# Performance work log

Measured on AMD Instinct MI355X. Metric: run time of the kernel, lower is better.

The kernel has to match this reference:

```python
import jax, jax.numpy as jnp
import numpy as np
from jax import lax

KS = 3
N = KS * KS  # 9 sampling locations per output pixel


def conv2d(x, w, b, pad, dil=1):
    out = lax.conv_general_dilated(
        x, w, window_strides=(1, 1), padding=((pad, pad), (pad, pad)),
        rhs_dilation=(dil, dil), dimension_numbers=('NCHW', 'OIHW', 'NCHW'))
    return out + b[None, :, None, None]


def deform_conv(x, p_w, p_b, dw, db):
    # Pure deform-conv-v2 semantics: offsets from p_conv, bilinear gather on
    # zero-padded input, then 3x3 contraction over the 9 gathered samples.
    B, C, H, W = x.shape
    offset = conv2d(x, p_w, p_b, 1)                       # (B, 2N, H, W)
    xp = jnp.pad(x, ((0, 0), (0, 0), (1, 1), (1, 1)))     # zero pad by 1
    Hp, Wp = H + 2, W + 2
    rr = jnp.arange(-(KS // 2), KS // 2 + 1)
    pi, pj = jnp.meshgrid(rr, rr, indexing='ij')
    p_n = jnp.concatenate([pi.reshape(-1), pj.reshape(-1)]).astype(x.dtype)   # (2N,)
    gi, gj = jnp.meshgrid(jnp.arange(1, H + 1), jnp.arange(1, W + 1), indexing='ij')
    p0 = jnp.concatenate([jnp.broadcast_to(gi, (N, H, W)),
                          jnp.broadcast_to(gj, (N, H, W))], 0).astype(x.dtype)  # (2N,H,W)
    p = p0[None] + p_n[None, :, None, None] + offset      # (B, 2N, H, W)
    p = jnp.transpose(p, (0, 2, 3, 1))                    # (B, H, W, 2N)
    py, px = p[..., :N], p[..., N:]
    fy, fx = jnp.floor(py), jnp.floor(px)
    lt_y = jnp.clip(fy, 0, Hp - 1); lt_x = jnp.clip(fx, 0, Wp - 1)
    rb_y = jnp.clip(fy + 1, 0, Hp - 1); rb_x = jnp.clip(fx + 1, 0, Wp - 1)
    pyc = jnp.clip(py, 0, Hp - 1); pxc = jnp.clip(px, 0, Wp - 1)
    g_lt = (1 + (lt_y - pyc)) * (1 + (lt_x - pxc))
    g_rb = (1 - (rb_y - pyc)) * (1 - (rb_x - pxc))
    g_lb = (1 + (lt_y - pyc)) * (1 - (rb_x - pxc))
    g_rt = (1 - (rb_y - pyc)) * (1 + (lt_x - pxc))
    xf = xp.reshape(B, C, Hp * Wp)

    def gather(qy, qx):
        idx = (qy.astype(jnp.int32) * Wp + qx.astype(jnp.int32)).reshape(B, -1)
        g = jax.vmap(lambda xb, ib: jnp.take(xb, ib, axis=1))(xf, idx)
        return g.reshape(B, C, H, W, N)

    x_lt = gather(lt_y, lt_x); x_rb = gather(rb_y, rb_x)
    x_lb = gather(lt_y, rb_x); x_rt = gather(rb_y, lt_x)
    samples = (g_lt[:, None] * x_lt + g_rb[:, None] * x_rb
               + g_lb[:, None] * x_lb + g_rt[:, None] * x_rt)  # (B,C,H,W,N)
    out = jnp.einsum('bchwn,ocn->bohw', samples, dw.reshape(dw.shape[0], C, N))
    return out + db[None, :, None, None]


def reference(x, w1, b1, w2, b2, w3, b3, w4, b4, p_w, p_b, dw, db, cw, cb):
    branches = [(w1, b1, 1, 1.0), (w2, b2, 3, 3.0), (w3, b3, 5, 5.0), (w4, b4, 7, 7.0)]
    feats = [deform_conv(conv2d(x, w, b, d, d) * s, p_w, p_b, dw, db)
             for (w, b, d, s) in branches]
    combined = jnp.concatenate(feats, axis=1)             # (B, 4*Cout, H, W)
    return jax.nn.relu(conv2d(combined, cw, cb, 0))


def setup_inputs() -> dict:
    B, Cin, Cout, H, W = 4, 128, 64, 128, 128
    key = jax.random.key(0)
    ks = jax.random.split(key, 16)
    sc3 = 1.0 / np.sqrt(Cin * 9)      # fan-in scale for 3x3 convs
    sc1 = 1.0 / np.sqrt(4 * Cout)     # fan-in scale for 1x1 fuse conv
    scd = 1.0 / np.sqrt(Cout * 9)     # deform main conv
    inp = {'x': jax.random.normal(ks[0], (B, Cin, H, W), jnp.float32)}
    for i in range(4):
        inp[f'w{i+1}'] = jax.random.normal(ks[1 + i], (Cout, Cin, 3, 3), jnp.float32) * sc3
        inp[f'b{i+1}'] = jax.random.normal(ks[5 + i], (Cout,), jnp.float32) * 0.01
    inp['p_w'] = jax.random.normal(ks[9], (2 * N, Cout, 3, 3), jnp.float32) * 0.01
    inp['p_b'] = jax.random.normal(ks[10], (2 * N,), jnp.float32) * 0.01
    inp['dw'] = jax.random.normal(ks[11], (Cout, Cout, 3, 3), jnp.float32) * scd
    inp['db'] = jax.random.normal(ks[12], (Cout,), jnp.float32) * 0.01
    inp['cw'] = jax.random.normal(ks[13], (Cout, 4 * Cout, 1, 1), jnp.float32) * sc1
    inp['cb'] = jax.random.normal(ks[14], (Cout,), jnp.float32) * 0.01
    return inp
```

## Files before the change

kernel.cpp:

```cpp
#include <hip/hip_runtime.h>
#include <hip/hip_bf16.h>

#define H 128
#define W 128
#define CIN 128
#define COUT 64
#define HW (H*W)
#define XW 130
#define FSL (XW*XW*64)
#define XTD 144

typedef __hip_bfloat16 bf16;
typedef __attribute__((ext_vector_type(8)))  short s16x8;
typedef __attribute__((ext_vector_type(16))) float f32x16;

__device__ __forceinline__ float b2f(bf16 v){ return __bfloat162float(v); }
__device__ __forceinline__ bf16  f2b(float v){ return __float2bfloat16(v); }
__device__ __forceinline__ unsigned pack2(float a, float b){
    unsigned short ua = __builtin_bit_cast(unsigned short, f2b(a));
    unsigned short ub = __builtin_bit_cast(unsigned short, f2b(b));
    return (unsigned)ua | ((unsigned)ub << 16);
}
__device__ __forceinline__ unsigned short b16u(float v){
    return __builtin_bit_cast(unsigned short, f2b(v));
}
__device__ __forceinline__ float2 up2(unsigned u){
    float lo = __builtin_bit_cast(float, u << 16);
    float hi = __builtin_bit_cast(float, u & 0xFFFF0000u);
    return make_float2(lo, hi);
}

__global__ __launch_bounds__(256) void k_prep(
    const float* __restrict__ w1, const float* __restrict__ w2,
    const float* __restrict__ w3, const float* __restrict__ w4,
    const float* __restrict__ dw, const float* __restrict__ cw,
    const float* __restrict__ pw,
    uint4* __restrict__ xt4, unsigned* __restrict__ wbt,
    unsigned* __restrict__ dwb2, unsigned* __restrict__ cwb2,
    unsigned* __restrict__ pwb)
{
    int bid = blockIdx.x;
    int t = threadIdx.x;
    if (bid < 1024){
        const int n4 = (4*XTD*XTD*64)/4;
        for (int i = bid*256 + t; i < n4; i += 1024*256)
            xt4[i] = make_uint4(0,0,0,0);
    } else if (bid < 1600){
        int tid = (bid-1024)*256 + t;
        int cpl = tid & 7;
        int oc  = (tid >> 3) & 63;
        int tap = (tid >> 9) % 9;
        int cg  = (tid / 4608) & 7;
        int d   = tid / 36864;
        const float* wt = (d==0)?w1:(d==1)?w2:(d==2)?w3:w4;
        int c = cg*8 + cpl;
        wbt[tid] = pack2(wt[((size_t)oc*CIN + 2*c  )*9 + tap],
                         wt[((size_t)oc*CIN + 2*c+1)*9 + tap]);
    } else if (bid < 1672){
        int i = (bid-1600)*256 + t;
        int n = i>>11, oc = (i>>5)&63, cp = i&31;
        dwb2[i] = pack2(dw[((size_t)oc*64 + 2*cp  )*9 + n],
                        dw[((size_t)oc*64 + 2*cp+1)*9 + n]);
    } else if (bid < 1704){
        int i = (bid-1672)*256 + t;
        int oc = i>>7, cp = i&127;
        cwb2[i] = pack2(cw[(size_t)oc*256 + 2*cp], cw[(size_t)oc*256 + 2*cp+1]);
    } else {
        int i = (bid-1704)*256 + t;
        int cl = i & 3, oc = (i>>2)&31, hf = (i>>7)&1, cq = (i>>8)&3, tap = i>>10;
        int c = cq*16 + hf*8 + cl*2;
        unsigned v = 0u;
        if (oc < 18)
            v = pack2(pw[((size_t)oc*64 + c  )*9 + tap],
                      pw[((size_t)oc*64 + c+1)*9 + tap]);
        pwb[i] = v;
    }
}

__global__ __launch_bounds__(256) void k_xprep(
    const float* __restrict__ x, unsigned* __restrict__ xt)
{
    int y = blockIdx.x, b = blockIdx.y;
    int t = threadIdx.x;
    __shared__ float xsm[64*131];
    for (int ci0 = 0; ci0 < 128; ci0 += 64){
        for (int i=0;i<32;i++){
            int idx = t + 256*i;
            int col = idx & 127, ci = idx >> 7;
            xsm[ci*131 + col] = x[(((size_t)b*CIN + ci0+ci)*H + y)*W + col];
        }
        __syncthreads();
        for (int i=0;i<16;i++){
            int idx = t + 256*i;
            int cpg = idx & 31, col = idx >> 5;
            int cgg = (ci0 >> 4) + (cpg >> 3);
            int cpl = cpg & 7;
            unsigned u = pack2(xsm[(2*cpg)*131 + col], xsm[(2*cpg+1)*131 + col]);
            xt[((((size_t)b*8 + cgg)*XTD + y+8)*XTD + col+8)*8 + cpl] = u;
        }
        __syncthreads();
    }
}

__global__ __launch_bounds__(256,2) void k_branch_mfma(
    const unsigned* __restrict__ xt, const unsigned* __restrict__ wbt,
    const float* __restrict__ b1, const float* __restrict__ b2,
    const float* __restrict__ b3, const float* __restrict__ b4,
    bf16* __restrict__ feats2)
{
    int bid = blockIdx.x;
    int xcd = bid & 7;
    int j   = bid >> 3;
    int zb  = xcd + 8*(j & 1);
    int hp  = j >> 1;
    int d = zb >> 2, b = zb & 3;
    int dil = 2*d + 1;
    int h0 = hp*2;
    const float* bs = (d==0)?b1:(d==1)?b2:(d==2)?b3:b4;
    const float scale = (float)dil;

    __shared__ unsigned smem[10368 + 6912];
    unsigned* As = smem;
    unsigned* Bs = smem + 10368;
    const unsigned short* As16 = (const unsigned short*)As;
    const unsigned short* Bs16 = (const unsigned short*)Bs;

    int t = threadIdx.x;
    int lane = t & 63;
    int w = t >> 6;
    int l31 = lane & 31;
    int half = lane >> 5;

    bf16* fb = feats2 + (size_t)zb*FSL;
    if (t < 32){
        int yy = h0 + 1 + (t>>4);
        int side = (t>>3)&1;
        int q = t & 7;
        uint4 z = make_uint4(0,0,0,0);
        *(uint4*)((unsigned short*)fb + ((size_t)yy*XW + side*129)*64 + q*8) = z;
    }
    if (hp == 0){
        uint4 z = make_uint4(0,0,0,0);
        for (int i=t; i<2080; i+=256){
            int row = i / 1040;
            int r = i % 1040;
            int xx = r >> 3, q = r & 7;
            *(uint4*)((unsigned short*)fb + ((size_t)(row*129)*XW + xx)*64 + q*8) = z;
        }
    }

    f32x16 acc[2][2];
    #pragma unroll
    for (int i=0;i<2;i++)
      #pragma unroll
      for (int jj=0;jj<2;jj++)
        #pragma unroll
        for (int e=0;e<16;e++) acc[i][jj][e] = 0.f;

    const unsigned* xtb_b = xt + (size_t)b*8*XTD*XTD*8;
    int r = w >> 1;
    int pxb = (w & 1) * 64;

    for (int cg=0; cg<8; cg++){
        const unsigned* xs_cg = xtb_b + (size_t)cg*XTD*XTD*8;
        #pragma unroll
        for (int i=0;i<7;i++){
            int idx4 = t + 256*i;
            if (idx4 < 1728){
                int cp4 = idx4 & 1;
                int s   = (idx4 >> 1) % 144;
                int row6= idx4 / 288;
                int ky = row6 >> 1, rr = row6 & 1;
                int yy = h0 + rr + (ky-1)*dil + 8;
                uint4 v = *(const uint4*)(xs_cg + ((size_t)yy*XTD + (s + 8 - dil))*8 + cp4*4);
                *(uint4*)&As[(row6*144 + s)*12 + cp4*4] = v;
            }
        }
        const unsigned* wb_cg = wbt + ((size_t)d*8 + cg)*4608;
        #pragma unroll
        for (int i=0;i<5;i++){
            int idx4 = t + 256*i;
            if (idx4 < 1152){
                int cp4 = idx4 & 1;
                int oc  = (idx4 >> 1) & 63;
                int tap = idx4 >> 7;
                uint4 v = *(const uint4*)(wb_cg + ((size_t)tap*64 + oc)*8 + cp4*4);
                *(uint4*)&Bs[(tap*64 + oc)*12 + cp4*4] = v;
            }
        }
        __syncthreads();
        #pragma unroll
        for (int tap=0; tap<9; tap++){
            int ky = tap/3, kx = tap%3;
            int rowb = (ky*2 + r)*144;
            s16x8 a0 = *(const s16x8*)(As16 + (rowb + pxb      + l31 + kx*dil)*24 + half*8);
            s16x8 a1 = *(const s16x8*)(As16 + (rowb + pxb + 32 + l31 + kx*dil)*24 + half*8);
            s16x8 bb0 = *(const s16x8*)(Bs16 + (tap*64      + l31)*24 + half*8);
            s16x8 bb1 = *(const s16x8*)(Bs16 + (tap*64 + 32 + l31)*24 + half*8);
            acc[0][0] = __builtin_amdgcn_mfma_f32_32x32x16_bf16(a0, bb0, acc[0][0], 0,0,0);
            acc[0][1] = __builtin_amdgcn_mfma_f32_32x32x16_bf16(a0, bb1, acc[0][1], 0,0,0);
            acc[1][0] = __builtin_amdgcn_mfma_f32_32x32x16_bf16(a1, bb0, acc[1][0], 0,0,0);
            acc[1][1] = __builtin_amdgcn_mfma_f32_32x32x16_bf16(a1, bb1, acc[1][1], 0,0,0);
        }
        __syncthreads();
    }

    unsigned short* ep = (unsigned short*)smem;
    float bias0 = bs[l31], bias1 = bs[32 + l31];
    #pragma unroll
    for (int i=0;i<2;i++){
      #pragma unroll
      for (int jj=0;jj<2;jj++){
        int oc = jj*32 + l31;
        float bj = jj ? bias1 : bias0;
        #pragma unroll
        for (int rg=0; rg<4; rg++){
            int m0 = 64*w + 32*i + 8*rg + 4*half;
            #pragma unroll
            for (int e=0;e<4;e++)
                ep[(m0+e)*64 + oc] = b16u((acc[i][jj][4*rg+e] + bj)*scale);
        }
      }
    }
    __syncthreads();
    {
        int row = t >> 7, pxm = t & 127;
        unsigned short* drow = (unsigned short*)fb + ((size_t)(h0+1+row)*XW + pxm + 1)*64;
        const unsigned short* srow = ep + t*64;
        #pragma unroll
        for (int q=0;q<8;q++)
            *(uint4*)(drow + q*8) = *(const uint4*)(srow + q*8);
    }
}

__global__ __launch_bounds__(256,2) void k_offset_mfma(
    const bf16* __restrict__ feats2,
    const unsigned* __restrict__ pwb,
    const float* __restrict__ pb,
    bf16* __restrict__ offs)
{
    int bid = blockIdx.x;
    int xcd  = bid & 7;
    int h    = (bid >> 3) & 127;
    int pass = bid >> 10;
    int zb   = xcd + 8*pass;

    int t = threadIdx.x;
    int lane = t & 63, w = t >> 6;
    int l31 = lane & 31, half = lane >> 5;

    __shared__ unsigned short xs[3*132*68];

    const unsigned short* fin = (const unsigned short*)(feats2 + (size_t)zb*FSL);
    for (int i=t; i<3120; i+=256){
        int row = i / 1040;
        int r   = i % 1040;
        int col = r >> 3, q = r & 7;
        uint4 v = *(const uint4*)(fin + ((size_t)(h+row)*XW + col)*64 + q*8);
        *(uint4*)&xs[(row*132 + col)*68 + q*8] = v;
    }
    __syncthreads();

    f32x16 acc;
    #pragma unroll
    for (int e=0;e<16;e++) acc[e] = 0.f;

    int pxw = 32*w + l31;
    #pragma unroll
    for (int tap=0; tap<9; tap++){
        int ky = tap/3, kx = tap%3;
        const unsigned short* arow = &xs[(ky*132 + pxw + kx)*68 + half*8];
        const unsigned* brow = pwb + (((size_t)tap*4)*2 + half)*128 + l31*4;
        #pragma unroll
        for (int cq=0; cq<4; cq++){
            s16x8 a  = *(const s16x8*)(arow + cq*16);
            s16x8 b0 = *(const s16x8*)(brow + cq*256);
            acc = __builtin_amdgcn_mfma_f32_32x32x16_bf16(a, b0, acc, 0,0,0);
        }
    }
    __syncthreads();

    unsigned short* ep = (unsigned short*)xs;
    if (l31 < 18){
        float bias = pb[l31];
        #pragma unroll
        for (int rg=0; rg<4; rg++){
            int m0 = 32*w + 4*half + 8*rg;
            #pragma unroll
            for (int e=0;e<4;e++)
                ep[l31*132 + m0+e] = b16u(acc[4*rg+e] + bias);
        }
    }
    __syncthreads();
    unsigned short* obase = (unsigned short*)(offs + (size_t)zb*18*HW) ;
    for (int i=t; i<288; i+=256){
        int oc = i >> 4, sg = i & 15;
        *(uint4*)(obase + (size_t)oc*HW + h*W + sg*8) = *(const uint4*)(ep + oc*132 + sg*8);
    }
}

__global__ __launch_bounds__(256,4) void k_deform_mfma(
    const bf16* __restrict__ feats2,
    const bf16* __restrict__ offs,
    const unsigned* __restrict__ dwb2,
    const float* __restrict__ db,
    bf16* __restrict__ dout2)
{
    int bid = blockIdx.x;
    int xcd  = bid & 7;
    int h    = (bid >> 3) & 127;
    int pass = bid >> 10;
    int zb   = xcd + 8*pass;

    int t = threadIdx.x;
    int lane = t & 63, w = t >> 6;
    int l31 = lane & 31, half = lane >> 5;
    int pxg = t >> 3;
    int cq  = t & 7;
    int sub_w = cq >> 1;
    int hf8   = cq & 1;

    #define AROW 516
    __shared__ unsigned smem_d[8*AROW + 2304 + 1024];
    unsigned* Asu = smem_d;
    unsigned* Bsu = smem_d + 8*AROW;
    unsigned* Cd  = smem_d + 8*AROW + 2304;

    const bf16* obase = offs + (size_t)zb*18*HW + h*W;
    const unsigned short* fbase = (const unsigned short*)(feats2 + (size_t)zb*FSL);

    f32x16 acc0, acc1;
    #pragma unroll
    for (int e=0;e<16;e++){ acc0[e]=0.f; acc1[e]=0.f; }

    for (int n=0; n<9; n++){
        const uint4* dsrc = (const uint4*)(dwb2 + n*2048);
        #pragma unroll
        for (int i=0;i<2;i++){
            int j = t + 256*i;
            int idx4 = j*4;
            int oc = idx4 >> 5, cp = idx4 & 31;
            *(uint4*)&Bsu[oc*36 + cp] = dsrc[j];
        }
        if (t < 128){
            float offy = b2f(obase[n*HW + t]);
            float offx = b2f(obase[(n+9)*HW + t]);
            float py  = (float)(h + n/3) + offy;
            float pxf = (float)(t + n%3) + offx;
            float fy = floorf(py), fx = floorf(pxf);
            float lty = fminf(fmaxf(fy,     0.f),129.f);
            float ltx = fminf(fmaxf(fx,     0.f),129.f);
            float rby = fminf(fmaxf(fy+1.f, 0.f),129.f);
            float rbx = fminf(fmaxf(fx+1.f, 0.f),129.f);
            float pyc = fminf(fmaxf(py,     0.f),129.f);
            float pxc = fminf(fmaxf(pxf,    0.f),129.f);
            float ay = 1.f + (lty-pyc), by = 1.f - (rby-pyc);
            float ax = 1.f + (ltx-pxc), bx = 1.f - (rbx-pxc);
            unsigned* cp = &Cd[t*8];
            cp[0] = __builtin_bit_cast(unsigned, ay*ax);
            cp[1] = __builtin_bit_cast(unsigned, ay*bx);
            cp[2] = __builtin_bit_cast(unsigned, by*ax);
            cp[3] = __builtin_bit_cast(unsigned, by*bx);
            cp[4] = (unsigned)(((int)lty*XW + (int)ltx)*64);
            cp[5] = (unsigned)(((int)rbx - (int)ltx)*64);
            cp[6] = (unsigned)(((int)rby - (int)lty)*XW*64);
        }
        __syncthreads();
        #pragma unroll
        for (int s=0; s<4; s++){
            int px = s*32 + pxg;
            const unsigned* cp = &Cd[px*8];
            uint4 c0 = *(const uint4*)cp;
            uint4 c1 = *(const uint4*)(cp + 4);
            float glt = __builtin_bit_cast(float, c0.x);
            float glb = __builtin_bit_cast(float, c0.y);
            float grt = __builtin_bit_cast(float, c0.z);
            float grb = __builtin_bit_cast(float, c0.w);
            int base = (int)c1.x;
            int dxo  = (int)c1.y;
            int dyo  = (int)c1.z;

            const unsigned short* fc = fbase + base + cq*8;
            unsigned LT[4], LB[4], RT[4], RB[4];
            *(uint4*)LT = *(const uint4*)(fc);
            *(uint4*)LB = *(const uint4*)(fc+dxo);
            *(uint4*)RT = *(const uint4*)(fc+dyo);
            *(uint4*)RB = *(const uint4*)(fc+dyo+dxo);
            unsigned pk[4];
            #pragma unroll
            for (int jq=0;jq<4;jq++){
                float2 a = up2(LT[jq]), bq = up2(LB[jq]);
                float2 c = up2(RT[jq]), dq = up2(RB[jq]);
                float slo = glt*a.x + glb*bq.x + grt*c.x + grb*dq.x;
                float shi = glt*a.y + glb*bq.y + grt*c.y + grb*dq.y;
                pk[jq] = pack2(slo, shi);
            }
            uint4 av; av.x=pk[0]; av.y=pk[1]; av.z=pk[2]; av.w=pk[3];
            *(uint4*)&Asu[(sub_w*2 + hf8)*AROW + px*4] = av;
        }
        __syncthreads();
        const unsigned short* As16 = (const unsigned short*)Asu;
        const unsigned short* Bs16 = (const unsigned short*)Bsu;
        #pragma unroll
        for (int s=0;s<4;s++){
            s16x8 a  = *(const s16x8*)(As16 + (s*2+half)*(AROW*2) + (32*w + l31)*8);
            s16x8 b0 = *(const s16x8*)(Bs16 + (l31*36 + s*8 + half*4)*2);
            s16x8 b1 = *(const s16x8*)(Bs16 + ((32+l31)*36 + s*8 + half*4)*2);
            acc0 = __builtin_amdgcn_mfma_f32_32x32x16_bf16(a, b0, acc0, 0,0,0);
            acc1 = __builtin_amdgcn_mfma_f32_32x32x16_bf16(a, b1, acc1, 0,0,0);
        }
        __syncthreads();
    }

    unsigned short* ep = (unsigned short*)smem_d;
    #pragma unroll
    for (int nt=0; nt<2; nt++){
        int oc = nt*32 + l31;
        float bias = db[oc];
        const f32x16& A = nt ? acc1 : acc0;
        #pragma unroll
        for (int rg=0; rg<4; rg++){
            int m0 = 32*w + 4*half + 8*rg;
            #pragma unroll
            for (int e=0;e<4;e++)
                ep[(m0+e)*64 + oc] = b16u(A[4*rg+e] + bias);
        }
    }
    __syncthreads();
    uint4* dst = (uint4*)((unsigned short*)dout2 + ((size_t)zb*128 + h)*(128*64));
    #pragma unroll
    for (int i=0;i<4;i++)
        dst[t + 256*i] = ((const uint4*)ep)[t + 256*i];
    #undef AROW
}

__global__ __launch_bounds__(256,2) void k_combine_mfma(
    const bf16* __restrict__ dout2,
    const unsigned* __restrict__ cwb2,
    const float* __restrict__ cb,
    float* __restrict__ out)
{
    int h = blockIdx.x, b = blockIdx.y;
    int t = threadIdx.x;
    int px = t & 127, hf = t >> 7;
    int lane = t & 63, w = t >> 6, l31 = lane & 31, half = lane >> 5;

    __shared__ unsigned Bsu[64*132];
    __shared__ unsigned Asu2[1024];

    for (int i=t; i<8192; i+=256){
        int oc = i>>7, cp = i&127;
        Bsu[oc*132 + cp] = cwb2[i];
    }
    f32x16 acc0, acc1;
    #pragma unroll
    for (int e=0;e<16;e++){ acc0[e]=0.f; acc1[e]=0.f; }

    const unsigned short* dbase0 = (const unsigned short*)dout2;
    size_t rowsel = ((size_t)b*128 + h)*128 + px;
    uint4 v = *(const uint4*)(dbase0 + rowsel*64 + hf*8);
    for (int kc=0; kc<16; kc++){
        *(uint4*)&Asu2[(hf*128+px)*4] = v;
        __syncthreads();
        if (kc < 15){
            int kn = kc+1;
            int d = kn>>2, c16 = kn&3;
            v = *(const uint4*)(dbase0 + ((size_t)d*4*128*128*64 + rowsel*64) + c16*16 + hf*8);
        }
        const unsigned short* As16 = (const unsigned short*)Asu2;
        const unsigned short* Bs16 = (const unsigned short*)Bsu;
        s16x8 a  = *(const s16x8*)(As16 + (half*128 + 32*w + l31)*8);
        s16x8 b0 = *(const s16x8*)(Bs16 + (l31*132 + kc*8 + half*4)*2);
        s16x8 b1 = *(const s16x8*)(Bs16 + ((32+l31)*132 + kc*8 + half*4)*2);
        acc0 = __builtin_amdgcn_mfma_f32_32x32x16_bf16(a, b0, acc0, 0,0,0);
        acc1 = __builtin_amdgcn_mfma_f32_32x32x16_bf16(a, b1, acc1, 0,0,0);
        __syncthreads();
    }
    float* ep = (float*)Bsu;
    #pragma unroll
    for (int nt=0; nt<2; nt++){
        int oc = nt*32 + l31;
        float bias = cb[oc];
        const f32x16& A = nt ? acc1 : acc0;
        #pragma unroll
        for (int rg=0; rg<4; rg++){
            int m0 = 32*w + 4*half + 8*rg;
            #pragma unroll
            for (int e=0;e<4;e++)
                ep[oc*132 + m0+e] = fmaxf(A[4*rg+e] + bias, 0.f);
        }
    }
    __syncthreads();
    for (int i=t; i<2048; i+=256){
        int oc = i>>5, sg = i&31;
        *(uint4*)&out[(((size_t)b*64+oc)*128 + h)*128 + sg*4] = *(const uint4*)&ep[oc*132 + sg*4];
    }
}

extern "C" void kernel_launch(void* const* d_in, const int* in_sizes, int n_in,
                              void* d_out, int out_size, void* d_ws, size_t ws_size,
                              hipStream_t stream) {
    const float* x  = (const float*)d_in[0];
    const float* w1 = (const float*)d_in[1];
    const float* b1 = (const float*)d_in[2];
    const float* w2 = (const float*)d_in[3];
    const float* b2 = (const float*)d_in[4];
    const float* w3 = (const float*)d_in[5];
    const float* b3 = (const float*)d_in[6];
    const float* w4 = (const float*)d_in[7];
    const float* b4 = (const float*)d_in[8];
    const float* pw = (const float*)d_in[9];
    const float* pb = (const float*)d_in[10];
    const float* dw = (const float*)d_in[11];
    const float* db = (const float*)d_in[12];
    const float* cw = (const float*)d_in[13];
    const float* cb = (const float*)d_in[14];
    float* out = (float*)d_out;

    bf16* feats2 = (bf16*)d_ws;
    bf16* offs   = feats2 + (size_t)16*FSL;
    bf16* region2 = offs + (size_t)16*18*HW;
    bf16* dout2  = region2;
    unsigned* xt  = (unsigned*)region2;
    unsigned* wbt = xt + (size_t)4*8*XTD*XTD*8;
    unsigned* dwb2 = (unsigned*)(dout2 + (size_t)16*128*128*64);
    unsigned* cwb2 = dwb2 + 18432;
    unsigned* pwb  = cwb2 + 8192;

    k_prep        <<<dim3(1740),    256, 0, stream>>>(w1,w2,w3,w4, dw, cw, pw,
                                                      (uint4*)xt, wbt, dwb2, cwb2, pwb);
    k_xprep       <<<dim3(128,4),   256, 0, stream>>>(x, xt);
    k_branch_mfma <<<dim3(1024),    256, 0, stream>>>(xt, wbt, b1,b2,b3,b4, feats2);
    k_offset_mfma <<<dim3(2048),    256, 0, stream>>>(feats2, pwb, pb, offs);
    k_deform_mfma <<<dim3(2048),    256, 0, stream>>>(feats2, offs, dwb2, db, dout2);
    k_combine_mfma<<<dim3(128,4),   256, 0, stream>>>(dout2, cwb2, cb, out);
}
```

Baseline: 316.3 us.

## Pipeline deform gather: double-buffer coords, prefetch corners, read weights from global

The deform-conv kernel now computes the bilinear coordinates for the next tap into a second LDS buffer while the current tap is processed. This removes one barrier per tap. Corner loads for the next 32-pixel slice are issued before blending the current one, and the blend uses packed two-wide float math. The MFMA B operand is read straight from global memory instead of being staged in LDS, which cuts LDS use and a store pass but relies on cache for weight reuse and adds register pressure.

```diff
diff --git a/kernel.cpp b/kernel.cpp
--- a/kernel.cpp
+++ b/kernel.cpp
@@ -13,6 +13,7 @@
 typedef __hip_bfloat16 bf16;
 typedef __attribute__((ext_vector_type(8)))  short s16x8;
 typedef __attribute__((ext_vector_type(16))) float f32x16;
+typedef __attribute__((ext_vector_type(2)))  float f32x2;
 
 __device__ __forceinline__ float b2f(bf16 v){ return __bfloat162float(v); }
 __device__ __forceinline__ bf16  f2b(float v){ return __float2bfloat16(v); }
@@ -28,6 +29,12 @@
     float lo = __builtin_bit_cast(float, u << 16);
     float hi = __builtin_bit_cast(float, u & 0xFFFF0000u);
     return make_float2(lo, hi);
+}
+__device__ __forceinline__ f32x2 up2v(unsigned u){
+    f32x2 r;
+    r.x = __builtin_bit_cast(float, u << 16);
+    r.y = __builtin_bit_cast(float, u & 0xFFFF0000u);
+    return r;
 }
 
 __global__ __launch_bounds__(256) void k_prep(
@@ -299,6 +306,31 @@
     }
 }
 
+__device__ __forceinline__ void deform_coords(
+    const bf16* __restrict__ obase, int h, int n, int px, unsigned* cp)
+{
+    float offy = b2f(obase[n*HW + px]);
+    float offx = b2f(obase[(n+9)*HW + px]);
+    float py  = (float)(h + n/3) + offy;
+    float pxf = (float)(px + n%3) + offx;
+    float fy = floorf(py), fx = floorf(pxf);
+    float lty = fminf(fmaxf(fy,     0.f),129.f);
+    float ltx = fminf(fmaxf(fx,     0.f),129.f);
+    float rby = fminf(fmaxf(fy+1.f, 0.f),129.f);
+    float rbx = fminf(fmaxf(fx+1.f, 0.f),129.f);
+    float pyc = fminf(fmaxf(py,     0.f),129.f);
+    float pxc = fminf(fmaxf(pxf,    0.f),129.f);
+    float ay = 1.f + (lty-pyc), by = 1.f - (rby-pyc);
+    float ax = 1.f + (ltx-pxc), bx = 1.f - (rbx-pxc);
+    cp[0] = __builtin_bit_cast(unsigned, ay*ax);
+    cp[1] = __builtin_bit_cast(unsigned, ay*bx);
+    cp[2] = __builtin_bit_cast(unsigned, by*ax);
+    cp[3] = __builtin_bit_cast(unsigned, by*bx);
+    cp[4] = (unsigned)(((int)lty*XW + (int)ltx)*64);
+    cp[5] = (unsigned)(((int)rbx - (int)ltx)*64);
+    cp[6] = (unsigned)(((int)rby - (int)lty)*XW*64);
+}
+
 __global__ __launch_bounds__(256,4) void k_deform_mfma(
     const bf16* __restrict__ feats2,
     const bf16* __restrict__ offs,
@@ -321,10 +353,9 @@
     int hf8   = cq & 1;
 
     #define AROW 516
-    __shared__ unsigned smem_d[8*AROW + 2304 + 1024];
+    __shared__ unsigned smem_d[8*AROW + 2048];
     unsigned* Asu = smem_d;
-    unsigned* Bsu = smem_d + 8*AROW;
-    unsigned* Cd  = smem_d + 8*AROW + 2304;
+    unsigned* Cd  = smem_d + 8*AROW;
 
     const bf16* obase = offs + (size_t)zb*18*HW + h*W;
     const unsigned short* fbase = (const unsigned short*)(feats2 + (size_t)zb*FSL);
@@ -333,79 +364,78 @@
     #pragma unroll
     for (int e=0;e<16;e++){ acc0[e]=0.f; acc1[e]=0.f; }
 
+    if (t < 128) deform_coords(obase, h, 0, t, &Cd[t*8]);
+    __syncthreads();
+
+    unsigned LTv[2][4], LBv[2][4], RTv[2][4], RBv[2][4];
+    float wg[2][4];
+
     for (int n=0; n<9; n++){
-        const uint4* dsrc = (const uint4*)(dwb2 + n*2048);
-        #pragma unroll
-        for (int i=0;i<2;i++){
-            int j = t + 256*i;
-            int idx4 = j*4;
-            int oc = idx4 >> 5, cp = idx4 & 31;
-            *(uint4*)&Bsu[oc*36 + cp] = dsrc[j];
-        }
-        if (t < 128){
-            float offy = b2f(obase[n*HW + t]);
-            float offx = b2f(obase[(n+9)*HW + t]);
-            float py  = (float)(h + n/3) + offy;
-            float pxf = (float)(t + n%3) + offx;
-            float fy = floorf(py), fx = floorf(pxf);
-            float lty = fminf(fmaxf(fy,     0.f),129.f);
-            float ltx = fminf(fmaxf(fx,     0.f),129.f);
-            float rby = fminf(fmaxf(fy+1.f, 0.f),129.f);
-            float rbx = fminf(fmaxf(fx+1.f, 0.f),129.f);
-            float pyc = fminf(fmaxf(py,     0.f),129.f);
-            float pxc = fminf(fmaxf(pxf,    0.f),129.f);
-            float ay = 1.f + (lty-pyc), by = 1.f - (rby-pyc);
-            float ax = 1.f + (ltx-pxc), bx = 1.f - (rbx-pxc);
-            unsigned* cp = &Cd[t*8];
-            cp[0] = __builtin_bit_cast(unsigned, ay*ax);
-            cp[1] = __builtin_bit_cast(unsigned, ay*bx);
-            cp[2] = __builtin_bit_cast(unsigned, by*ax);
-            cp[3] = __builtin_bit_cast(unsigned, by*bx);
-            cp[4] = (unsigned)(((int)lty*XW + (int)ltx)*64);
-            cp[5] = (unsigned)(((int)rbx - (int)ltx)*64);
-            cp[6] = (unsigned)(((int)rby - (int)lty)*XW*64);
-        }
-        __syncthreads();
-        #pragma unroll
-        for (int s=0; s<4; s++){
-            int px = s*32 + pxg;
-            const unsigned* cp = &Cd[px*8];
+        const unsigned* Cdc = Cd + (n&1)*1024;
+        unsigned*       Cdn = Cd + ((n+1)&1)*1024;
+
+        {
+            const unsigned* cp = &Cdc[(pxg)*8];
             uint4 c0 = *(const uint4*)cp;
             uint4 c1 = *(const uint4*)(cp + 4);
-            float glt = __builtin_bit_cast(float, c0.x);
-            float glb = __builtin_bit_cast(float, c0.y);
-            float grt = __builtin_bit_cast(float, c0.z);
-            float grb = __builtin_bit_cast(float, c0.w);
-            int base = (int)c1.x;
-            int dxo  = (int)c1.y;
-            int dyo  = (int)c1.z;
-
-            const unsigned short* fc = fbase + base + cq*8;
-            unsigned LT[4], LB[4], RT[4], RB[4];
-            *(uint4*)LT = *(const uint4*)(fc);
-            *(uint4*)LB = *(const uint4*)(fc+dxo);
-            *(uint4*)RT = *(const uint4*)(fc+dyo);
-            *(uint4*)RB = *(const uint4*)(fc+dyo+dxo);
+            wg[0][0] = __builtin_bit_cast(float, c0.x);
+            wg[0][1] = __builtin_bit_cast(float, c0.y);
+            wg[0][2] = __builtin_bit_cast(float, c0.z);
+            wg[0][3] = __builtin_bit_cast(float, c0.w);
+            int dxo = (int)c1.y, dyo = (int)c1.z;
+            const unsigned short* fc = fbase + (int)c1.x + cq*8;
+            *(uint4*)&LTv[0][0] = *(const uint4*)(fc);
+            *(uint4*)&LBv[0][0] = *(const uint4*)(fc+dxo);
+            *(uint4*)&RTv[0][0] = *(const uint4*)(fc+dyo);
+            *(uint4*)&RBv[0][0] = *(const uint4*)(fc+dyo+dxo);
+        }
+        if (n < 8 && t < 128) deform_coords(obase, h, n+1, t, &Cdn[t*8]);
+
+        #pragma unroll
+        for (int s=0; s<4; s++){
+            const int par = s & 1;
+            if (s < 3){
+                const int nx = par ^ 1;
+                const unsigned* cp = &Cdc[((s+1)*32+pxg)*8];
+                uint4 c0 = *(const uint4*)cp;
+                uint4 c1 = *(const uint4*)(cp + 4);
+                wg[nx][0] = __builtin_bit_cast(float, c0.x);
+                wg[nx][1] = __builtin_bit_cast(float, c0.y);
+                wg[nx][2] = __builtin_bit_cast(float, c0.z);
+                wg[nx][3] = __builtin_bit_cast(float, c0.w);
+                int dxo = (int)c1.y, dyo = (int)c1.z;
+                const unsigned short* fc = fbase + (int)c1.x + cq*8;
+                *(uint4*)&LTv[nx][0] = *(const uint4*)(fc);
+                *(uint4*)&LBv[nx][0] = *(const uint4*)(fc+dxo);
+                *(uint4*)&RTv[nx][0] = *(const uint4*)(fc+dyo);
+                *(uint4*)&RBv[nx][0] = *(const uint4*)(fc+dyo+dxo);
+            }
+            f32x2 wlt = {wg[par][0], wg[par][0]};
+            f32x2 wlb = {wg[par][1], wg[par][1]};
+            f32x2 wrt = {wg[par][2], wg[par][2]};
+            f32x2 wrb = {wg[par][3], wg[par][3]};
             unsigned pk[4];
             #pragma unroll
-            for (int jq=0;jq<4;jq++){
-                float2 a = up2(LT[jq]), bq = up2(LB[jq]);
-                float2 c = up2(RT[jq]), dq = up2(RB[jq]);
-                float slo = glt*a.x + glb*bq.x + grt*c.x + grb*dq.x;
-                float shi = glt*a.y + glb*bq.y + grt*c.y + grb*dq.y;
-                pk[jq] = pack2(slo, shi);
+            for (int jq=0; jq<4; jq++){
+                f32x2 r = wlt * up2v(LTv[par][jq]);
+                r += wlb * up2v(LBv[par][jq]);
+                r += wrt * up2v(RTv[par][jq]);
+                r += wrb * up2v(RBv[par][jq]);
+                pk[jq] = pack2(r.x, r.y);
             }
+            int px = s*32 + pxg;
             uint4 av; av.x=pk[0]; av.y=pk[1]; av.z=pk[2]; av.w=pk[3];
             *(uint4*)&Asu[(sub_w*2 + hf8)*AROW + px*4] = av;
         }
         __syncthreads();
+
         const unsigned short* As16 = (const unsigned short*)Asu;
-        const unsigned short* Bs16 = (const unsigned short*)Bsu;
-        #pragma unroll
-        for (int s=0;s<4;s++){
+        const unsigned short* dnb  = (const unsigned short*)(dwb2 + n*2048);
+        #pragma unroll
+        for (int s=0; s<4; s++){
             s16x8 a  = *(const s16x8*)(As16 + (s*2+half)*(AROW*2) + (32*w + l31)*8);
-            s16x8 b0 = *(const s16x8*)(Bs16 + (l31*36 + s*8 + half*4)*2);
-            s16x8 b1 = *(const s16x8*)(Bs16 + ((32+l31)*36 + s*8 + half*4)*2);
+            s16x8 b0 = *(const s16x8*)(dnb + (l31*32      + s*8 + half*4)*2);
+            s16x8 b1 = *(const s16x8*)(dnb + ((32+l31)*32 + s*8 + half*4)*2);
             acc0 = __builtin_amdgcn_mfma_f32_32x32x16_bf16(a, b0, acc0, 0,0,0);
             acc1 = __builtin_amdgcn_mfma_f32_32x32x16_bf16(a, b1, acc1, 0,0,0);
         }
```

After: 352.9 us. +11.6%, slower.

## Compute deform samples directly in MFMA operand registers, remove LDS staging

Applied to the files above, without the earlier changes.

The deform kernel now has each lane compute its own pixel's bilinear coordinates and gather the channel slice that maps straight onto its MFMA A-fragment. Weight B-fragments are loaded directly from global memory instead of being staged through LDS. This removes the shared-memory staging of coefficients, samples and weights, and the three barriers per tap. In exchange, the coordinate math is repeated per lane and B-fragments come from global memory or cache with no shared reuse.

```diff
diff --git a/kernel.cpp b/kernel.cpp
--- a/kernel.cpp
+++ b/kernel.cpp
@@ -315,104 +315,68 @@
     int t = threadIdx.x;
     int lane = t & 63, w = t >> 6;
     int l31 = lane & 31, half = lane >> 5;
-    int pxg = t >> 3;
-    int cq  = t & 7;
-    int sub_w = cq >> 1;
-    int hf8   = cq & 1;
-
-    #define AROW 516
-    __shared__ unsigned smem_d[8*AROW + 2304 + 1024];
-    unsigned* Asu = smem_d;
-    unsigned* Bsu = smem_d + 8*AROW;
-    unsigned* Cd  = smem_d + 8*AROW + 2304;
+    int px  = 32*w + l31;
+    int chb = half*8;
+
+    __shared__ unsigned short ep[8192];
 
     const bf16* obase = offs + (size_t)zb*18*HW + h*W;
     const unsigned short* fbase = (const unsigned short*)(feats2 + (size_t)zb*FSL);
+    int boff0 = l31*64 + half*8;
+    int boff1 = boff0 + 2048;
 
     f32x16 acc0, acc1;
     #pragma unroll
     for (int e=0;e<16;e++){ acc0[e]=0.f; acc1[e]=0.f; }
 
     for (int n=0; n<9; n++){
-        const uint4* dsrc = (const uint4*)(dwb2 + n*2048);
-        #pragma unroll
-        for (int i=0;i<2;i++){
-            int j = t + 256*i;
-            int idx4 = j*4;
-            int oc = idx4 >> 5, cp = idx4 & 31;
-            *(uint4*)&Bsu[oc*36 + cp] = dsrc[j];
-        }
-        if (t < 128){
-            float offy = b2f(obase[n*HW + t]);
-            float offx = b2f(obase[(n+9)*HW + t]);
-            float py  = (float)(h + n/3) + offy;
-            float pxf = (float)(t + n%3) + offx;
-            float fy = floorf(py), fx = floorf(pxf);
-            float lty = fminf(fmaxf(fy,     0.f),129.f);
-            float ltx = fminf(fmaxf(fx,     0.f),129.f);
-            float rby = fminf(fmaxf(fy+1.f, 0.f),129.f);
-            float rbx = fminf(fmaxf(fx+1.f, 0.f),129.f);
-            float pyc = fminf(fmaxf(py,     0.f),129.f);
-            float pxc = fminf(fmaxf(pxf,    0.f),129.f);
-            float ay = 1.f + (lty-pyc), by = 1.f - (rby-pyc);
-            float ax = 1.f + (ltx-pxc), bx = 1.f - (rbx-pxc);
-            unsigned* cp = &Cd[t*8];
-            cp[0] = __builtin_bit_cast(unsigned, ay*ax);
-            cp[1] = __builtin_bit_cast(unsigned, ay*bx);
-            cp[2] = __builtin_bit_cast(unsigned, by*ax);
-            cp[3] = __builtin_bit_cast(unsigned, by*bx);
-            cp[4] = (unsigned)(((int)lty*XW + (int)ltx)*64);
-            cp[5] = (unsigned)(((int)rbx - (int)ltx)*64);
-            cp[6] = (unsigned)(((int)rby - (int)lty)*XW*64);
-        }
-        __syncthreads();
+        const unsigned short* dnb16 = (const unsigned short*)(dwb2 + n*2048);
+
+        float offy = b2f(obase[n*HW + px]);
+        float offx = b2f(obase[(n+9)*HW + px]);
+        float py  = (float)(h + n/3) + offy;
+        float pxf = (float)(px + n%3) + offx;
+        float fy = floorf(py), fx = floorf(pxf);
+        float lty = fminf(fmaxf(fy,     0.f),129.f);
+        float ltx = fminf(fmaxf(fx,     0.f),129.f);
+        float rby = fminf(fmaxf(fy+1.f, 0.f),129.f);
+        float rbx = fminf(fmaxf(fx+1.f, 0.f),129.f);
+        float pyc = fminf(fmaxf(py,     0.f),129.f);
+        float pxc = fminf(fmaxf(pxf,    0.f),129.f);
+        float ay = 1.f + (lty-pyc), by = 1.f - (rby-pyc);
+        float ax = 1.f + (ltx-pxc), bx = 1.f - (rbx-pxc);
+        float glt = ay*ax, glb = ay*bx, grt = by*ax, grb = by*bx;
+        int base = ((int)lty*XW + (int)ltx)*64;
+        int dxo  = ((int)rbx - (int)ltx)*64;
+        int dyo  = ((int)rby - (int)lty)*XW*64;
+        const unsigned short* fc = fbase + base + chb;
+
         #pragma unroll
         for (int s=0; s<4; s++){
-            int px = s*32 + pxg;
-            const unsigned* cp = &Cd[px*8];
-            uint4 c0 = *(const uint4*)cp;
-            uint4 c1 = *(const uint4*)(cp + 4);
-            float glt = __builtin_bit_cast(float, c0.x);
-            float glb = __builtin_bit_cast(float, c0.y);
-            float grt = __builtin_bit_cast(float, c0.z);
-            float grb = __builtin_bit_cast(float, c0.w);
-            int base = (int)c1.x;
-            int dxo  = (int)c1.y;
-            int dyo  = (int)c1.z;
-
-            const unsigned short* fc = fbase + base + cq*8;
+            s16x8 bf0 = *(const s16x8*)(dnb16 + boff0 + s*16);
+            s16x8 bf1 = *(const s16x8*)(dnb16 + boff1 + s*16);
+            const unsigned short* f0 = fc + s*16;
             unsigned LT[4], LB[4], RT[4], RB[4];
-            *(uint4*)LT = *(const uint4*)(fc);
-            *(uint4*)LB = *(const uint4*)(fc+dxo);
-            *(uint4*)RT = *(const uint4*)(fc+dyo);
-            *(uint4*)RB = *(const uint4*)(fc+dyo+dxo);
+            *(uint4*)LT = *(const uint4*)(f0);
+            *(uint4*)LB = *(const uint4*)(f0+dxo);
+            *(uint4*)RT = *(const uint4*)(f0+dyo);
+            *(uint4*)RB = *(const uint4*)(f0+dyo+dxo);
             unsigned pk[4];
             #pragma unroll
             for (int jq=0;jq<4;jq++){
-                float2 a = up2(LT[jq]), bq = up2(LB[jq]);
-                float2 c = up2(RT[jq]), dq = up2(RB[jq]);
-                float slo = glt*a.x + glb*bq.x + grt*c.x + grb*dq.x;
-                float shi = glt*a.y + glb*bq.y + grt*c.y + grb*dq.y;
+                float2 a2 = up2(LT[jq]), b2 = up2(LB[jq]);
+                float2 c2 = up2(RT[jq]), d2 = up2(RB[jq]);
+                float slo = glt*a2.x + glb*b2.x + grt*c2.x + grb*d2.x;
+                float shi = glt*a2.y + glb*b2.y + grt*c2.y + grb*d2.y;
                 pk[jq] = pack2(slo, shi);
             }
             uint4 av; av.x=pk[0]; av.y=pk[1]; av.z=pk[2]; av.w=pk[3];
-            *(uint4*)&Asu[(sub_w*2 + hf8)*AROW + px*4] = av;
-        }
-        __syncthreads();
-        const unsigned short* As16 = (const unsigned short*)Asu;
-        const unsigned short* Bs16 = (const unsigned short*)Bsu;
-        #pragma unroll
-        for (int s=0;s<4;s++){
-            s16x8 a  = *(const s16x8*)(As16 + (s*2+half)*(AROW*2) + (32*w + l31)*8);
-            s16x8 b0 = *(const s16x8*)(Bs16 + (l31*36 + s*8 + half*4)*2);
-            s16x8 b1 = *(const s16x8*)(Bs16 + ((32+l31)*36 + s*8 + half*4)*2);
-            acc0 = __builtin_amdgcn_mfma_f32_32x32x16_bf16(a, b0, acc0, 0,0,0);
-            acc1 = __builtin_amdgcn_mfma_f32_32x32x16_bf16(a, b1, acc1, 0,0,0);
-        }
-        __syncthreads();
-    }
-
-    unsigned short* ep = (unsigned short*)smem_d;
+            s16x8 afr = __builtin_bit_cast(s16x8, av);
+            acc0 = __builtin_amdgcn_mfma_f32_32x32x16_bf16(afr, bf0, acc0, 0,0,0);
+            acc1 = __builtin_amdgcn_mfma_f32_32x32x16_bf16(afr, bf1, acc1, 0,0,0);
+        }
+    }
+
     #pragma unroll
     for (int nt=0; nt<2; nt++){
         int oc = nt*32 + l31;
@@ -431,7 +395,6 @@
     #pragma unroll
     for (int i=0;i<4;i++)
         dst[t + 256*i] = ((const uint4*)ep)[t + 256*i];
-    #undef AROW
 }
 
 __global__ __launch_bounds__(256,2) void k_combine_mfma(
```

New measurement: 441.0 us. +39.4%, slower.
